# Kernel optimization log

Hardware: AMD Instinct MI355X
Metric: run time of the kernel (lower is better)

Reference implementation:

```python
import jax, jax.numpy as jnp
import numpy as np

_FP8_MAX = 448.0  # finfo(float8_e4m3fn).max


def _quantize_fp8(w):
    """Per-tensor FP8 quantization: returns fp8-snapped weight (as f32) and scale."""
    scale = jnp.maximum(jnp.max(jnp.abs(w)).astype(jnp.float32) / _FP8_MAX, 1e-12)
    w_q = (w / scale).astype(jnp.float8_e4m3fn).astype(jnp.float32)
    return w_q, scale


def setup_inputs() -> dict:
    key = jax.random.key(0)
    k_x, k_g, k_u, k_d = jax.random.split(key, 4)
    B, S, H, I = 4, 2048, 4096, 11008
    x = jax.random.normal(k_x, (B, S, H), dtype=jnp.float32)
    gate = jax.random.normal(k_g, (I, H), dtype=jnp.float32) * 0.05
    up = jax.random.normal(k_u, (I, H), dtype=jnp.float32) * 0.05
    down = jax.random.normal(k_d, (H, I), dtype=jnp.float32) * 0.05
    gate_w, gate_w_scale = _quantize_fp8(gate)
    up_w, up_w_scale = _quantize_fp8(up)
    down_w, down_w_scale = _quantize_fp8(down)
    one = jnp.float32(1.0)
    return {
        "x": x,
        "gate_w": gate_w, "up_w": up_w, "down_w": down_w,
        "gate_w_scale": gate_w_scale, "up_w_scale": up_w_scale, "down_w_scale": down_w_scale,
        "gate_in_scale": one, "up_in_scale": one, "down_in_scale": one,
    }


def _fake_quant_fp8_linear(x, w_q, in_scale, w_scale):
    # Fake-quantize activations to FP8 (per-tensor scale), dequantize weight, GEMM.
    x_q = jnp.clip(x / in_scale, -_FP8_MAX, _FP8_MAX)
    x_dq = x_q.astype(jnp.float8_e4m3fn).astype(jnp.float32) * in_scale
    w_dq = w_q * w_scale  # w_q values are already on the FP8 grid
    return jnp.einsum('bsh,ih->bsi', x_dq, w_dq)


def reference(x, gate_w, up_w, down_w, gate_w_scale, up_w_scale, down_w_scale,
              gate_in_scale, up_in_scale, down_in_scale):
    gate_out = _fake_quant_fp8_linear(x, gate_w, gate_in_scale, gate_w_scale)
    up_out = _fake_quant_fp8_linear(x, up_w, up_in_scale, up_w_scale)
    hidden = jax.nn.silu(gate_out) * up_out  # SwiGLU
    return _fake_quant_fp8_linear(hidden, down_w, down_in_scale, down_w_scale)
```

## Files before the change

### kernel.cpp

```cpp
#include <hip/hip_runtime.h>
#include <stdint.h>


typedef float f32x4 __attribute__((ext_vector_type(4)));
typedef int   i32x4 __attribute__((ext_vector_type(4)));
typedef int   i32x8 __attribute__((ext_vector_type(8)));
typedef unsigned int u32;

#define AS1 __attribute__((address_space(1)))
#define AS3 __attribute__((address_space(3)))

#define TM 128
#define TN 128
#define BKB 128

#define SCALE1 0x7F7F7F7F

__device__ __forceinline__ void gld_lds16(const uint8_t* g, uint8_t* l) {
  __builtin_amdgcn_global_load_lds((const AS1 u32*)g, (AS3 u32*)l, 16, 0, 0);
}

__device__ __forceinline__ uint8_t f32_to_fp8(float v) {
  v = fminf(fmaxf(v, -448.f), 448.f);
  int r = __builtin_amdgcn_cvt_pk_fp8_f32(v, v, 0, false);
  return (uint8_t)(r & 0xff);
}

__device__ __forceinline__ i32x8 read_frag32(const uint8_t* s, int row, int ko, int swz) {
  const uint8_t* p = s + row * BKB;
  i32x4 lo = *(const i32x4*)(p + ((ko) ^ swz));
  i32x4 hi = *(const i32x4*)(p + ((ko + 16) ^ swz));
  return __builtin_shufflevector(lo, hi, 0, 1, 2, 3, 4, 5, 6, 7);
}

__global__ __launch_bounds__(256) void quant_fp8_k(const float* __restrict__ in,
                                                   uint8_t* __restrict__ out,
                                                   const float* __restrict__ scale_ptr,
                                                   long n8) {
  long i = (long)blockIdx.x * 256 + threadIdx.x;
  if (i >= n8) return;
  float inv = scale_ptr ? (1.0f / scale_ptr[0]) : 1.0f;
  const float4* p = (const float4*)(in + i * 8);
  float4 a = p[0], b = p[1];
  float v0 = fminf(fmaxf(a.x * inv, -448.f), 448.f);
  float v1 = fminf(fmaxf(a.y * inv, -448.f), 448.f);
  float v2 = fminf(fmaxf(a.z * inv, -448.f), 448.f);
  float v3 = fminf(fmaxf(a.w * inv, -448.f), 448.f);
  float v4 = fminf(fmaxf(b.x * inv, -448.f), 448.f);
  float v5 = fminf(fmaxf(b.y * inv, -448.f), 448.f);
  float v6 = fminf(fmaxf(b.z * inv, -448.f), 448.f);
  float v7 = fminf(fmaxf(b.w * inv, -448.f), 448.f);
  int lo = __builtin_amdgcn_cvt_pk_fp8_f32(v0, v1, 0, false);
  lo = __builtin_amdgcn_cvt_pk_fp8_f32(v2, v3, lo, true);
  int hi = __builtin_amdgcn_cvt_pk_fp8_f32(v4, v5, 0, false);
  hi = __builtin_amdgcn_cvt_pk_fp8_f32(v6, v7, hi, true);
  ((int2*)out)[i] = make_int2(lo, hi);
}

__global__ __launch_bounds__(256, 2) void gemm1_swiglu(
    const uint8_t* __restrict__ Xq,
    const uint8_t* __restrict__ Gq,
    const uint8_t* __restrict__ Uq,
    uint8_t* __restrict__ Hq,
    const float* __restrict__ gws, const float* __restrict__ uws,
    const float* __restrict__ gis, const float* __restrict__ uis,
    const float* __restrict__ dis,
    int M, int H, int I) {
  __shared__ uint8_t sX[TM * BKB];
  __shared__ uint8_t sG[TN * BKB];
  __shared__ uint8_t sU[TN * BKB];

  const int tid = threadIdx.x;
  const int wave = tid >> 6, lane = tid & 63;
  const int wr = wave >> 1, wc = wave & 1;
  const int lrow = lane & 15;
  const int lkg = lane >> 4;
  const int swz = (lrow & 7) << 4;
  const int ko = lkg * 32;

  const int GX = 43, GY = 16;
  const int per = GX * GY;
  const int g = blockIdx.x & 7;
  const int w = blockIdx.x >> 3;
  const int ggx = g & 1, ggy = g >> 1;
  const int xb = ggx * GX + w / GY;
  const int yb = ggy * GY + (w % GY);
  const int bM = yb * TM, bN = xb * TN;

  f32x4 accG[4][4] = {};
  f32x4 accU[4][4] = {};

  const uint8_t* gx = Xq + (size_t)bM * H;
  const uint8_t* gg = Gq + (size_t)bN * H;
  const uint8_t* gu = Uq + (size_t)bN * H;

  for (int k0 = 0; k0 < H; k0 += BKB) {
    if (k0) __syncthreads();
#pragma unroll
    for (int it = 0; it < 4; ++it) {
      int c = it * 256 + tid;
      int r = c >> 3;
      int col = ((c & 7) ^ (r & 7)) * 16;
      size_t go = (size_t)r * H + k0 + col;
      int lo = (it * 4 + wave) * 1024;
      gld_lds16(gx + go, sX + lo);
      gld_lds16(gg + go, sG + lo);
      gld_lds16(gu + go, sU + lo);
    }
    asm volatile("s_waitcnt vmcnt(0)" ::: "memory");
    __syncthreads();

    i32x8 af[4];
#pragma unroll
    for (int i = 0; i < 4; ++i)
      af[i] = read_frag32(sX, wr * 64 + i * 16 + lrow, ko, swz);
#pragma unroll
    for (int j = 0; j < 4; ++j) {
      i32x8 gf = read_frag32(sG, wc * 64 + j * 16 + lrow, ko, swz);
      i32x8 uf = read_frag32(sU, wc * 64 + j * 16 + lrow, ko, swz);
#pragma unroll
      for (int i = 0; i < 4; ++i) {
        accG[i][j] = __builtin_amdgcn_mfma_scale_f32_16x16x128_f8f6f4(
            af[i], gf, accG[i][j], 0, 0, 0, SCALE1, 0, SCALE1);
        accU[i][j] = __builtin_amdgcn_mfma_scale_f32_16x16x128_f8f6f4(
            af[i], uf, accU[i][j], 0, 0, 0, SCALE1, 0, SCALE1);
      }
    }
  }

  const float sg = gws[0] * gis[0];
  const float su = uws[0] * uis[0];
  const float invd = 1.0f / dis[0];

  __syncthreads();
  uint8_t* sH = sX;

#pragma unroll
  for (int i = 0; i < 4; ++i)
#pragma unroll
    for (int j = 0; j < 4; ++j)
#pragma unroll
      for (int t = 0; t < 4; ++t) {
        float g2 = accG[i][j][t] * sg;
        float u = accU[i][j][t] * su;
        float h = (g2 / (1.0f + expf(-g2))) * u * invd;
        int row = wr * 64 + i * 16 + lkg * 4 + t;
        int col = wc * 64 + j * 16 + lrow;
        sH[row * TN + col] = f32_to_fp8(h);
      }
  __syncthreads();
#pragma unroll
  for (int it = 0; it < 4; ++it) {
    int o = (it * 256 + tid) * 16;
    int row = o >> 7, col = o & 127;
    *(int4*)(Hq + (size_t)(bM + row) * I + bN + col) = *(const int4*)(sH + o);
  }
}

__global__ __launch_bounds__(256, 2) void gemm2_down(
    const uint8_t* __restrict__ Hq,
    const uint8_t* __restrict__ Dq,
    float* __restrict__ Out,
    const float* __restrict__ dws, const float* __restrict__ dis,
    int M, int I, int Hd) {
  __shared__ uint8_t sA[TM * BKB];
  __shared__ uint8_t sB[2 * TN * BKB];

  const int tid = threadIdx.x;
  const int wave = tid >> 6, lane = tid & 63;
  const int wr = wave >> 1, wc = wave & 1;
  const int lrow = lane & 15;
  const int lkg = lane >> 4;
  const int swz = (lrow & 7) << 4;
  const int ko = lkg * 32;

  const int L = (blockIdx.x & 7) * 128 + (blockIdx.x >> 3);
  const int g = L >> 8, w = L & 255;
  const int xb = w >> 4;
  const int yb = (g << 4) + (w & 15);
  const int bM = yb * TM, bN = xb * 256;

  f32x4 acc[4][8] = {};

  const uint8_t* ga = Hq + (size_t)bM * I;
  const uint8_t* gb = Dq + (size_t)bN * I;

  for (int k0 = 0; k0 < I; k0 += BKB) {
    if (k0) __syncthreads();
#pragma unroll
    for (int it = 0; it < 4; ++it) {
      int c = it * 256 + tid;
      int r = c >> 3;
      int col = ((c & 7) ^ (r & 7)) * 16;
      gld_lds16(ga + (size_t)r * I + k0 + col, sA + (it * 4 + wave) * 1024);
    }
#pragma unroll
    for (int it = 0; it < 8; ++it) {
      int c = it * 256 + tid;
      int r = c >> 3;
      int col = ((c & 7) ^ (r & 7)) * 16;
      gld_lds16(gb + (size_t)r * I + k0 + col, sB + (it * 4 + wave) * 1024);
    }
    asm volatile("s_waitcnt vmcnt(0)" ::: "memory");
    __syncthreads();

    i32x8 af[4];
#pragma unroll
    for (int i = 0; i < 4; ++i)
      af[i] = read_frag32(sA, wr * 64 + i * 16 + lrow, ko, swz);
#pragma unroll
    for (int j = 0; j < 8; ++j) {
      i32x8 bf = read_frag32(sB, wc * 128 + j * 16 + lrow, ko, swz);
#pragma unroll
      for (int i = 0; i < 4; ++i)
        acc[i][j] = __builtin_amdgcn_mfma_scale_f32_16x16x128_f8f6f4(
            af[i], bf, acc[i][j], 0, 0, 0, SCALE1, 0, SCALE1);
    }
  }

  const float ds = dws[0] * dis[0];
#pragma unroll
  for (int i = 0; i < 4; ++i)
#pragma unroll
    for (int j = 0; j < 8; ++j) {
      int row = bM + wr * 64 + i * 16 + lkg * 4;
      int col = bN + wc * 128 + j * 16 + lrow;
#pragma unroll
      for (int t = 0; t < 4; ++t)
        Out[(size_t)(row + t) * Hd + col] = acc[i][j][t] * ds;
    }
}

extern "C" void kernel_launch(void* const* d_in, const int* in_sizes, int n_in,
                              void* d_out, int out_size, void* d_ws, size_t ws_size,
                              hipStream_t stream) {
  const float* x   = (const float*)d_in[0];
  const float* gw  = (const float*)d_in[1];
  const float* uw  = (const float*)d_in[2];
  const float* dw  = (const float*)d_in[3];
  const float* gws = (const float*)d_in[4];
  const float* uws = (const float*)d_in[5];
  const float* dws = (const float*)d_in[6];
  const float* gis = (const float*)d_in[7];
  const float* uis = (const float*)d_in[8];
  const float* dis = (const float*)d_in[9];

  const int Hd = 4096;
  const int M  = in_sizes[0] / Hd;
  const int I  = in_sizes[1] / Hd;

  const size_t szX = (size_t)M * Hd;
  const size_t szW = (size_t)I * Hd;
  const size_t szH = (size_t)M * I;

  uint8_t* xq = (uint8_t*)d_ws;
  uint8_t* gq = xq + szX;
  uint8_t* uq = gq + szW;
  uint8_t* hq = uq + szW;
  uint8_t* dq = gq;

  if (ws_size < szX + 2 * szW + szH) return;

  float* out = (float*)d_out;

  {
    long n8 = (long)(szX / 8);
    quant_fp8_k<<<dim3((n8 + 255) / 256), dim3(256), 0, stream>>>(x, xq, gis, n8);
  }
  {
    long n8 = (long)(szW / 8);
    quant_fp8_k<<<dim3((n8 + 255) / 256), dim3(256), 0, stream>>>(gw, gq, nullptr, n8);
    quant_fp8_k<<<dim3((n8 + 255) / 256), dim3(256), 0, stream>>>(uw, uq, nullptr, n8);
  }

  gemm1_swiglu<<<dim3((I / TN) * (M / TM)), dim3(256), 0, stream>>>(
      xq, gq, uq, hq, gws, uws, gis, uis, dis, M, Hd, I);

  {
    long n8 = (long)(szW / 8);
    quant_fp8_k<<<dim3((n8 + 255) / 256), dim3(256), 0, stream>>>(dw, dq, nullptr, n8);
  }
  gemm2_down<<<dim3((Hd / 256) * (M / TM)), dim3(256), 0, stream>>>(
      hq, dq, out, dws, dis, M, I, Hd);
}
```

Measured before the change: 1.211 ms.

## Enlarge gate/up GEMM tile to 256x128 with double-buffered LDS prefetch

```diff
diff --git a/kernel.cpp b/kernel.cpp
--- a/kernel.cpp
+++ b/kernel.cpp
@@ -12,6 +12,8 @@
 
 #define TM 128
 #define TN 128
+#define BM1 256
+#define BN1 128
 #define BKB 128
 
 #define SCALE1 0x7F7F7F7F
@@ -57,7 +59,7 @@
   ((int2*)out)[i] = make_int2(lo, hi);
 }
 
-__global__ __launch_bounds__(256, 2) void gemm1_swiglu(
+__global__ __launch_bounds__(512, 2) void gemm1_swiglu(
     const uint8_t* __restrict__ Xq,
     const uint8_t* __restrict__ Gq,
     const uint8_t* __restrict__ Uq,
@@ -66,9 +68,9 @@
     const float* __restrict__ gis, const float* __restrict__ uis,
     const float* __restrict__ dis,
     int M, int H, int I) {
-  __shared__ uint8_t sX[TM * BKB];
-  __shared__ uint8_t sG[TN * BKB];
-  __shared__ uint8_t sU[TN * BKB];
+  __shared__ uint8_t sX[2][BM1 * BKB];
+  __shared__ uint8_t sG[2][BN1 * BKB];
+  __shared__ uint8_t sU[2][BN1 * BKB];
 
   const int tid = threadIdx.x;
   const int wave = tid >> 6, lane = tid & 63;
@@ -78,14 +80,13 @@
   const int swz = (lrow & 7) << 4;
   const int ko = lkg * 32;
 
-  const int GX = 43, GY = 16;
-  const int per = GX * GY;
+  const int GX = 43, GY = 8;
   const int g = blockIdx.x & 7;
   const int w = blockIdx.x >> 3;
   const int ggx = g & 1, ggy = g >> 1;
   const int xb = ggx * GX + w / GY;
   const int yb = ggy * GY + (w % GY);
-  const int bM = yb * TM, bN = xb * TN;
+  const int bM = yb * BM1, bN = xb * BN1;
 
   f32x4 accG[4][4] = {};
   f32x4 accU[4][4] = {};
@@ -94,30 +95,55 @@
   const uint8_t* gg = Gq + (size_t)bN * H;
   const uint8_t* gu = Uq + (size_t)bN * H;
 
-  for (int k0 = 0; k0 < H; k0 += BKB) {
-    if (k0) __syncthreads();
-#pragma unroll
-    for (int it = 0; it < 4; ++it) {
-      int c = it * 256 + tid;
-      int r = c >> 3;
-      int col = ((c & 7) ^ (r & 7)) * 16;
-      size_t go = (size_t)r * H + k0 + col;
-      int lo = (it * 4 + wave) * 1024;
-      gld_lds16(gx + go, sX + lo);
-      gld_lds16(gg + go, sG + lo);
-      gld_lds16(gu + go, sU + lo);
-    }
-    asm volatile("s_waitcnt vmcnt(0)" ::: "memory");
-    __syncthreads();
+  auto stage_x = [&](int buf, int it, int k0) {
+    int c = it * 512 + tid;
+    int r = c >> 3;
+    int col = ((c & 7) ^ (r & 7)) * 16;
+    gld_lds16(gx + (size_t)r * H + k0 + col, &sX[buf][(it * 8 + wave) * 1024]);
+  };
+  auto stage_g = [&](int buf, int it, int k0) {
+    int c = it * 512 + tid;
+    int r = c >> 3;
+    int col = ((c & 7) ^ (r & 7)) * 16;
+    gld_lds16(gg + (size_t)r * H + k0 + col, &sG[buf][(it * 8 + wave) * 1024]);
+  };
+  auto stage_u = [&](int buf, int it, int k0) {
+    int c = it * 512 + tid;
+    int r = c >> 3;
+    int col = ((c & 7) ^ (r & 7)) * 16;
+    gld_lds16(gu + (size_t)r * H + k0 + col, &sU[buf][(it * 8 + wave) * 1024]);
+  };
+
+  const int NK = H / BKB;
+
+  stage_x(0, 0, 0); stage_x(0, 1, 0); stage_x(0, 2, 0); stage_x(0, 3, 0);
+  stage_g(0, 0, 0); stage_g(0, 1, 0); stage_u(0, 0, 0); stage_u(0, 1, 0);
+
+  for (int t = 0; t < NK; ++t) {
+    const int cur = t & 1, nxt = cur ^ 1;
+    const int k1 = (t + 1) * BKB;
+    const bool pre = (t + 1 < NK);
+
+    if (pre) { stage_x(nxt, 0, k1); stage_g(nxt, 0, k1); }
+    if (pre) asm volatile("s_waitcnt vmcnt(2)" ::: "memory");
+    else     asm volatile("s_waitcnt vmcnt(0)" ::: "memory");
+    __builtin_amdgcn_s_barrier();
 
     i32x8 af[4];
 #pragma unroll
     for (int i = 0; i < 4; ++i)
-      af[i] = read_frag32(sX, wr * 64 + i * 16 + lrow, ko, swz);
+      af[i] = read_frag32(&sX[cur][0], wr * 64 + i * 16 + lrow, ko, swz);
+
 #pragma unroll
     for (int j = 0; j < 4; ++j) {
-      i32x8 gf = read_frag32(sG, wc * 64 + j * 16 + lrow, ko, swz);
-      i32x8 uf = read_frag32(sU, wc * 64 + j * 16 + lrow, ko, swz);
+      i32x8 gf = read_frag32(&sG[cur][0], wc * 64 + j * 16 + lrow, ko, swz);
+      i32x8 uf = read_frag32(&sU[cur][0], wc * 64 + j * 16 + lrow, ko, swz);
+      if (pre) {
+        if (j == 1)      { stage_x(nxt, 1, k1); stage_g(nxt, 1, k1); }
+        else if (j == 2) { stage_x(nxt, 2, k1); stage_u(nxt, 0, k1); }
+        else if (j == 3) { stage_x(nxt, 3, k1); stage_u(nxt, 1, k1); }
+      }
+      __builtin_amdgcn_s_setprio(1);
 #pragma unroll
       for (int i = 0; i < 4; ++i) {
         accG[i][j] = __builtin_amdgcn_mfma_scale_f32_16x16x128_f8f6f4(
@@ -125,33 +151,35 @@
         accU[i][j] = __builtin_amdgcn_mfma_scale_f32_16x16x128_f8f6f4(
             af[i], uf, accU[i][j], 0, 0, 0, SCALE1, 0, SCALE1);
       }
-    }
+      __builtin_amdgcn_s_setprio(0);
+    }
+    asm volatile("s_waitcnt lgkmcnt(0)" ::: "memory");
+    __builtin_amdgcn_s_barrier();
   }
 
   const float sg = gws[0] * gis[0];
   const float su = uws[0] * uis[0];
   const float invd = 1.0f / dis[0];
 
-  __syncthreads();
-  uint8_t* sH = sX;
+  uint8_t* sH = &sX[0][0];
 
 #pragma unroll
   for (int i = 0; i < 4; ++i)
 #pragma unroll
     for (int j = 0; j < 4; ++j)
 #pragma unroll
-      for (int t = 0; t < 4; ++t) {
-        float g2 = accG[i][j][t] * sg;
-        float u = accU[i][j][t] * su;
+      for (int tt = 0; tt < 4; ++tt) {
+        float g2 = accG[i][j][tt] * sg;
+        float u = accU[i][j][tt] * su;
         float h = (g2 / (1.0f + expf(-g2))) * u * invd;
-        int row = wr * 64 + i * 16 + lkg * 4 + t;
+        int row = wr * 64 + i * 16 + lkg * 4 + tt;
         int col = wc * 64 + j * 16 + lrow;
-        sH[row * TN + col] = f32_to_fp8(h);
+        sH[row * BN1 + col] = f32_to_fp8(h);
       }
   __syncthreads();
 #pragma unroll
   for (int it = 0; it < 4; ++it) {
-    int o = (it * 256 + tid) * 16;
+    int o = (it * 512 + tid) * 16;
     int row = o >> 7, col = o & 127;
     *(int4*)(Hq + (size_t)(bM + row) * I + bN + col) = *(const int4*)(sH + o);
   }
@@ -174,8 +202,7 @@
   const int swz = (lrow & 7) << 4;
   const int ko = lkg * 32;
 
-  const int L = (blockIdx.x & 7) * 128 + (blockIdx.x >> 3);
-  const int g = L >> 8, w = L & 255;
+  const int g = blockIdx.x >> 8, w = blockIdx.x & 255;
   const int xb = w >> 4;
   const int yb = (g << 4) + (w & 15);
   const int bM = yb * TM, bN = xb * 256;
@@ -273,7 +300,7 @@
     quant_fp8_k<<<dim3((n8 + 255) / 256), dim3(256), 0, stream>>>(uw, uq, nullptr, n8);
   }
 
-  gemm1_swiglu<<<dim3((I / TN) * (M / TM)), dim3(256), 0, stream>>>(
+  gemm1_swiglu<<<dim3((I / BN1) * (M / BM1)), dim3(512), 0, stream>>>(
       xq, gq, uq, hq, gws, uws, gis, uis, dis, M, Hd, I);
 
   {
```

Measured after the change: 1.467 ms. +21.1%, slower.
